# Optimization experiments

Measured on AMD Instinct MI355X. Metric: run time of the kernel, lower is better.

The kernel has to match this reference:

```python
import jax, jax.numpy as jnp
import numpy as np

N_NODES = 100000
N_EDGES = 1200000
D = 64          # hidden_feat_dim == out_feat_dim
D_CELL = 16     # cell_feat_dim
HID = 256       # MLP hidden width (from MLP(..., 256, ...))
N_TGT = 50000


def setup_inputs() -> dict:
    key = jax.random.key(0)
    ks = jax.random.split(key, 13)
    inv = lambda d: 1.0 / np.sqrt(d)
    return {
        "h": jax.random.normal(ks[0], (N_NODES, D), jnp.float32),
        "cell_feat": jax.random.normal(ks[1], (N_NODES, D_CELL), jnp.float32),
        "src": jax.random.randint(ks[2], (N_EDGES,), 0, N_NODES, jnp.int32),
        "dst": jax.random.randint(ks[3], (N_EDGES,), 0, N_NODES, jnp.int32),
        "targets": jax.random.randint(ks[4], (N_TGT,), 0, N_NODES, jnp.int32),
        "Wn1": jax.random.normal(ks[5], (D, HID), jnp.float32) * inv(D),
        "bn1": jnp.zeros((HID,), jnp.float32),
        "Wn2": jax.random.normal(ks[6], (HID, D), jnp.float32) * inv(HID),
        "bn2": jnp.zeros((D,), jnp.float32),
        "Ws1": jax.random.normal(ks[7], (D_CELL, HID), jnp.float32) * inv(D_CELL),
        "bs1": jnp.zeros((HID,), jnp.float32),
        "Ws2": jax.random.normal(ks[8], (HID, D), jnp.float32) * inv(HID),
        "bs2": jnp.zeros((D,), jnp.float32),
    }


def _mlp2(x, W1, b1, W2, b2):
    # MLP(d_in, 256, d_out) with LeakyReLU(negative_slope=0) == ReLU
    return jax.nn.relu(x @ W1 + b1) @ W2 + b2


def reference(h, cell_feat, src, dst, targets,
              Wn1, bn1, Wn2, bn2, Ws1, bs1, Ws2, bs2):
    # PathConv forward, even level_id > 0, flag_attn=False:
    #   pull(copy_src('h','m'), cell_msg_reduce, apply_cell_func) on 'cell' edges
    N = h.shape[0]
    m = h[src]  # gather edge messages [E, D]
    # cell_msg_reduce: per-dst, per-channel softmax over incoming messages
    mmax = jax.ops.segment_max(m, dst, num_segments=N)          # [N, D]
    mmax = jnp.where(jnp.isfinite(mmax), mmax, 0.0)             # isolated nodes
    e = jnp.exp(m - mmax[dst])                                  # [E, D]
    den = jax.ops.segment_sum(e, dst, num_segments=N)           # [N, D]
    num = jax.ops.segment_sum(e * m, dst, num_segments=N)       # sum(msg*softmax)
    h_neigh1 = num / jnp.where(den == 0.0, 1.0, den)            # [N, D]
    # apply_cell_func: fc_cell_self(cell_feat) + fc_cell_neigh(h_neigh1)
    h_new = _mlp2(cell_feat, Ws1, bs1, Ws2, bs2) + _mlp2(h_neigh1, Wn1, bn1, Wn2, bn2)
    h_new = jax.nn.relu(h_new)  # self.activation
    return h_new[targets]
```

## Files before the change

kernel.cpp:

```cpp
#include <hip/hip_runtime.h>

#define NN 100000
#define NE 1200000
#define DD 64
#define DC 16
#define DH 256
#define NT 50000
#define MAXDEG 64

typedef __attribute__((ext_vector_type(8))) short bf16x8;
typedef __attribute__((ext_vector_type(4))) short bf16x4;
typedef __attribute__((ext_vector_type(4))) float f32x4;

__device__ __forceinline__ unsigned short f2bf(float x) {
    unsigned int u = __float_as_uint(x);
    return (unsigned short)((u + 0x7FFFu + ((u >> 16) & 1u)) >> 16);
}
__device__ __forceinline__ float bf2f(unsigned short b) {
    return __uint_as_float(((unsigned int)b) << 16);
}

__device__ __forceinline__ void split8t(const float* p, bf16x8& hi, bf16x8& lo) {
    f32x4 a = *reinterpret_cast<const f32x4*>(p);
    f32x4 b = *reinterpret_cast<const f32x4*>(p + 4);
    #pragma unroll
    for (int j = 0; j < 4; ++j) {
        unsigned short h = (unsigned short)(__float_as_uint(a[j]) >> 16);
        hi[j] = (short)h;
        lo[j] = (short)(__float_as_uint(a[j] - bf2f(h)) >> 16);
    }
    #pragma unroll
    for (int j = 0; j < 4; ++j) {
        unsigned short h = (unsigned short)(__float_as_uint(b[j]) >> 16);
        hi[4 + j] = (short)h;
        lo[4 + j] = (short)(__float_as_uint(b[j] - bf2f(h)) >> 16);
    }
}

__device__ __forceinline__ bf16x8 zero8() {
    return bf16x8{0, 0, 0, 0, 0, 0, 0, 0};
}
__device__ __forceinline__ bf16x8 pad8(bf16x4 v) {
    return bf16x8{v[0], v[1], v[2], v[3], 0, 0, 0, 0};
}

#define N_W1NT 16384
#define N_W1ST 8192
#define N_W2N  16384
#define N_W2S  16384
#define N_PACK (N_W1NT + N_W1ST + N_W2N + N_W2S)
#define N_PREP NN

__global__ __launch_bounds__(256) void prep_k(
    const float* __restrict__ Wn1, const float* __restrict__ Ws1,
    const float* __restrict__ Wn2, const float* __restrict__ Ws2,
    unsigned short* __restrict__ W1nT, unsigned short* __restrict__ W1sT,
    unsigned short* __restrict__ W2n,  unsigned short* __restrict__ W2s,
    int* __restrict__ ifl, int* __restrict__ deg)
{
    int tid = blockIdx.x * 256 + threadIdx.x;
    if (tid < NN) ifl[tid] = -1;
    if (tid < NT + 16) deg[tid] = 0;
    if (tid >= N_PACK) return;
    float v; unsigned short* ph; int idx;
    if (tid < N_W1NT) {
        idx = tid;
        int j = idx & 7, l = (idx >> 3) & 63, rest = idx >> 9;
        int ks = rest & 1, c = rest >> 1;
        int feat = ks * 32 + ((l >> 4) << 3) + j, hid = (c << 4) + (l & 15);
        v = Wn1[(size_t)feat * DH + hid];
        ph = W1nT;
    } else if (tid < N_W1NT + N_W1ST) {
        idx = tid - N_W1NT;
        int j = idx & 7, l = (idx >> 3) & 63, c = idx >> 9;
        int k = ((l >> 4) << 3) + j, hid = (c << 4) + (l & 15);
        v = (k < DC) ? Ws1[(size_t)k * DH + hid] : 0.0f;
        ph = W1sT;
    } else if (tid < N_W1NT + N_W1ST + N_W2N) {
        idx = tid - N_W1NT - N_W1ST;
        int j = idx & 3, l = (idx >> 2) & 63, rest = idx >> 8;
        int u = rest & 3, c = rest >> 2;
        int row = (c << 4) + ((l >> 4) << 2) + j, col = (u << 4) + (l & 15);
        v = Wn2[(size_t)row * DD + col];
        ph = W2n;
    } else {
        idx = tid - N_W1NT - N_W1ST - N_W2N;
        int j = idx & 3, l = (idx >> 2) & 63, rest = idx >> 8;
        int u = rest & 3, c = rest >> 2;
        int row = (c << 4) + ((l >> 4) << 2) + j, col = (u << 4) + (l & 15);
        v = Ws2[(size_t)row * DD + col];
        ph = W2s;
    }
    ph[idx] = f2bf(v);
}

__global__ __launch_bounds__(256) void mark_wl_k(
    const int* __restrict__ tg, int* __restrict__ ifl, int* __restrict__ cnt)
{
    int i = blockIdx.x * 256 + threadIdx.x;
    int lane = threadIdx.x & 63;
    bool claim = false;
    int t = 0;
    if (i < NT) {
        t = tg[i];
        claim = (atomicCAS(&ifl[t], -1, -2) == -1);
    }
    unsigned long long mask = __ballot(claim);
    if (mask == 0ull) return;
    int nclaim = __popcll(mask);
    int leader = __ffsll((unsigned long long)mask) - 1;
    int base = 0;
    if (lane == leader) base = atomicAdd(cnt, nclaim);
    base = __shfl(base, leader);
    if (claim) {
        int rank = __popcll(mask & ((1ull << lane) - 1ull));
        ifl[t] = base + rank;
    }
}

#define NE4 (NE / 4)
#define N_SCAT (NE4 > NT ? NE4 : NT)

__global__ __launch_bounds__(256) void scatter_tgw_k(
    const int4* __restrict__ src4, const int4* __restrict__ dst4,
    const int* __restrict__ ifl, const int* __restrict__ tg,
    int* __restrict__ tgw, int* __restrict__ deg, int* __restrict__ csr)
{
    int tid = blockIdx.x * 256 + threadIdx.x;
    if (tid < NE4) {
        int4 d = dst4[tid];
        int4 s = src4[tid];
        int w;
        w = ifl[d.x]; if (w >= 0) { int sl = atomicAdd(&deg[w], 1); if (sl < MAXDEG) csr[w * MAXDEG + sl] = s.x; }
        w = ifl[d.y]; if (w >= 0) { int sl = atomicAdd(&deg[w], 1); if (sl < MAXDEG) csr[w * MAXDEG + sl] = s.y; }
        w = ifl[d.z]; if (w >= 0) { int sl = atomicAdd(&deg[w], 1); if (sl < MAXDEG) csr[w * MAXDEG + sl] = s.z; }
        w = ifl[d.w]; if (w >= 0) { int sl = atomicAdd(&deg[w], 1); if (sl < MAXDEG) csr[w * MAXDEG + sl] = s.w; }
    }
    if (tid < NT) tgw[tid] = ifl[tg[tid]];
}

__global__ __launch_bounds__(256) void reduce_k(
    const float* __restrict__ h, const int* __restrict__ csr,
    const int* __restrict__ deg, const int* __restrict__ cnt,
    float* __restrict__ hn_c)
{
    int gw = (blockIdx.x * 256 + threadIdx.x) >> 6;
    int lane = threadIdx.x & 63;
    if (gw >= cnt[0]) return;
    int g = min(deg[gw], MAXDEG);
    int sid = csr[gw * MAXDEG + lane];
    if (lane >= g) sid = 0;
    const int e4 = lane >> 4, c4 = lane & 15;

    f32x4 accd = {0.f, 0.f, 0.f, 0.f}, accn = {0.f, 0.f, 0.f, 0.f};
    for (int base = 0; base < g; base += 16) {
        f32x4 m[4];
        bool  val[4];
        #pragma unroll
        for (int bb = 0; bb < 4; ++bb) {
            int idx = base + bb * 4 + e4;
            val[bb] = (idx < g);
            if (base + bb * 4 < g) {
                int s = __shfl(sid, idx);
                m[bb] = *reinterpret_cast<const f32x4*>(
                            h + (size_t)s * DD + c4 * 4);
            } else {
                m[bb] = f32x4{0.f, 0.f, 0.f, 0.f};
                val[bb] = false;
            }
        }
        #pragma unroll
        for (int bb = 0; bb < 4; ++bb) {
            #pragma unroll
            for (int r = 0; r < 4; ++r) {
                float ex = __expf(m[bb][r]);
                ex = val[bb] ? ex : 0.f;
                accd[r] += ex;
                accn[r] = fmaf(ex, m[bb][r], accn[r]);
            }
        }
    }
    #pragma unroll
    for (int r = 0; r < 4; ++r) {
        accd[r] += __shfl_xor(accd[r], 16);
        accn[r] += __shfl_xor(accn[r], 16);
        accd[r] += __shfl_xor(accd[r], 32);
        accn[r] += __shfl_xor(accn[r], 32);
    }
    if (lane < 16) {
        f32x4 o;
        #pragma unroll
        for (int r = 0; r < 4; ++r)
            o[r] = (accd[r] == 0.f) ? 0.f : accn[r] / accd[r];
        *reinterpret_cast<f32x4*>(hn_c + (size_t)gw * DD + c4 * 4) = o;
    }
}

__global__ __launch_bounds__(256, 4) void mfma_mlp_k(
    const float* __restrict__ hn_c, const int* __restrict__ tgw,
    const float* __restrict__ cellf, const int* __restrict__ tg,
    const unsigned short* __restrict__ W1nT, const unsigned short* __restrict__ W1sT,
    const unsigned short* __restrict__ W2n,  const unsigned short* __restrict__ W2s,
    const float* __restrict__ bn1, const float* __restrict__ bs1,
    const float* __restrict__ bn2, const float* __restrict__ bs2,
    float* __restrict__ out)
{
    __shared__ float shbuf[4 * 16 * 68];
    float (*X)[84]      = reinterpret_cast<float(*)[84]>(shbuf);
    float (*Ys)[16][68] = reinterpret_cast<float(*)[16][68]>(shbuf);

    const int tid = threadIdx.x;
    const int wv = tid >> 6, ln = tid & 63;
    const int l16 = ln & 15, kb = (ln >> 4) << 3;
    const int rbase = blockIdx.x * 32;

    {
        int r = tid >> 3, seg = tid & 7;
        int row = rbase + r; if (row >= NT) row = NT - 1;
        int w = tgw[row];
        const float* hp = hn_c + (size_t)w * DD + seg * 8;
        *reinterpret_cast<f32x4*>(&X[r][seg * 8])     = *reinterpret_cast<const f32x4*>(hp);
        *reinterpret_cast<f32x4*>(&X[r][seg * 8 + 4]) = *reinterpret_cast<const f32x4*>(hp + 4);
        if (tid < 128) {
            int r2 = tid >> 2, q = tid & 3;
            int row2 = rbase + r2; if (row2 >= NT) row2 = NT - 1;
            int t2 = tg[row2];
            *reinterpret_cast<f32x4*>(&X[r2][64 + q * 4]) =
                *reinterpret_cast<const f32x4*>(cellf + (size_t)t2 * DC + q * 4);
        }
    }
    __syncthreads();

    bf16x8 xh[2][2], xl[2][2], sxh[2], sxl[2];
    #pragma unroll
    for (int g = 0; g < 2; ++g) {
        #pragma unroll
        for (int ks = 0; ks < 2; ++ks)
            split8t(&X[g * 16 + l16][ks * 32 + kb], xh[g][ks], xl[g][ks]);
        sxh[g] = zero8(); sxl[g] = zero8();
        if (ln < 32)
            split8t(&X[g * 16 + l16][64 + kb], sxh[g], sxl[g]);
    }
    __syncthreads();

    f32x4 accY[2][4];
    #pragma unroll
    for (int g = 0; g < 2; ++g)
        #pragma unroll
        for (int u = 0; u < 4; ++u) accY[g][u] = f32x4{0.f, 0.f, 0.f, 0.f};

    #pragma unroll
    for (int cc = 0; cc < 4; ++cc) {
        int cg = (wv << 2) + cc;
        f32x4 b1 = *reinterpret_cast<const f32x4*>(bn1 + cg * 16 + ((ln >> 4) << 2));
        f32x4 a1[2] = {b1, b1};
        #pragma unroll
        for (int ks = 0; ks < 2; ++ks) {
            bf16x8 wh = *reinterpret_cast<const bf16x8*>(W1nT + (((cg * 2 + ks) * 64 + ln) << 3));
            #pragma unroll
            for (int g = 0; g < 2; ++g) {
                a1[g] = __builtin_amdgcn_mfma_f32_16x16x32_bf16(wh, xh[g][ks], a1[g], 0, 0, 0);
                a1[g] = __builtin_amdgcn_mfma_f32_16x16x32_bf16(wh, xl[g][ks], a1[g], 0, 0, 0);
            }
        }
        bf16x8 pah[2], pal[2];
        #pragma unroll
        for (int g = 0; g < 2; ++g) {
            pah[g] = zero8(); pal[g] = zero8();
            #pragma unroll
            for (int r = 0; r < 4; ++r) {
                float d = fmaxf(a1[g][r], 0.f);
                unsigned short hh = (unsigned short)(__float_as_uint(d) >> 16);
                pah[g][r] = (short)hh;
                pal[g][r] = (short)(__float_as_uint(d - bf2f(hh)) >> 16);
            }
        }
        #pragma unroll
        for (int u = 0; u < 4; ++u) {
            bf16x8 wp = pad8(*reinterpret_cast<const bf16x4*>(W2n + (((cg * 4 + u) * 64 + ln) << 2)));
            #pragma unroll
            for (int g = 0; g < 2; ++g) {
                accY[g][u] = __builtin_amdgcn_mfma_f32_16x16x32_bf16(pah[g], wp, accY[g][u], 0, 0, 0);
                accY[g][u] = __builtin_amdgcn_mfma_f32_16x16x32_bf16(pal[g], wp, accY[g][u], 0, 0, 0);
            }
        }
    }

    #pragma unroll
    for (int cc = 0; cc < 4; ++cc) {
        int cg = (wv << 2) + cc;
        f32x4 b1 = *reinterpret_cast<const f32x4*>(bs1 + cg * 16 + ((ln >> 4) << 2));
        f32x4 a1[2] = {b1, b1};
        {
            bf16x8 wh = *reinterpret_cast<const bf16x8*>(W1sT + ((cg * 64 + ln) << 3));
            #pragma unroll
            for (int g = 0; g < 2; ++g) {
                a1[g] = __builtin_amdgcn_mfma_f32_16x16x32_bf16(wh, sxh[g], a1[g], 0, 0, 0);
                a1[g] = __builtin_amdgcn_mfma_f32_16x16x32_bf16(wh, sxl[g], a1[g], 0, 0, 0);
            }
        }
        bf16x8 pah[2], pal[2];
        #pragma unroll
        for (int g = 0; g < 2; ++g) {
            pah[g] = zero8(); pal[g] = zero8();
            #pragma unroll
            for (int r = 0; r < 4; ++r) {
                float d = fmaxf(a1[g][r], 0.f);
                unsigned short hh = (unsigned short)(__float_as_uint(d) >> 16);
                pah[g][r] = (short)hh;
                pal[g][r] = (short)(__float_as_uint(d - bf2f(hh)) >> 16);
            }
        }
        #pragma unroll
        for (int u = 0; u < 4; ++u) {
            bf16x8 wp = pad8(*reinterpret_cast<const bf16x4*>(W2s + (((cg * 4 + u) * 64 + ln) << 2)));
            #pragma unroll
            for (int g = 0; g < 2; ++g) {
                accY[g][u] = __builtin_amdgcn_mfma_f32_16x16x32_bf16(pah[g], wp, accY[g][u], 0, 0, 0);
                accY[g][u] = __builtin_amdgcn_mfma_f32_16x16x32_bf16(pal[g], wp, accY[g][u], 0, 0, 0);
            }
        }
    }

    #pragma unroll
    for (int g = 0; g < 2; ++g) {
        #pragma unroll
        for (int u = 0; u < 4; ++u)
            #pragma unroll
            for (int r = 0; r < 4; ++r)
                Ys[wv][(ln >> 4) * 4 + r][u * 16 + l16] = accY[g][u][r];
        __syncthreads();
        {
            int row = tid >> 4, cs = tid & 15;
            f32x4 s = {0.f, 0.f, 0.f, 0.f};
            #pragma unroll
            for (int wq = 0; wq < 4; ++wq)
                s += *reinterpret_cast<const f32x4*>(&Ys[wq][row][cs * 4]);
            f32x4 c0 = *reinterpret_cast<const f32x4*>(bn2 + cs * 4);
            f32x4 c1 = *reinterpret_cast<const f32x4*>(bs2 + cs * 4);
            #pragma unroll
            for (int j = 0; j < 4; ++j) s[j] = fmaxf(s[j] + c0[j] + c1[j], 0.f);
            int rowg = rbase + g * 16 + row;
            if (rowg < NT)
                *reinterpret_cast<f32x4*>(out + (size_t)rowg * DD + cs * 4) = s;
        }
        __syncthreads();
    }
}

extern "C" void kernel_launch(void* const* d_in, const int* in_sizes, int n_in,
                              void* d_out, int out_size, void* d_ws, size_t ws_size,
                              hipStream_t stream)
{
    const float* h     = (const float*)d_in[0];
    const float* cellf = (const float*)d_in[1];
    const int*   src   = (const int*)d_in[2];
    const int*   dst   = (const int*)d_in[3];
    const int*   tg    = (const int*)d_in[4];
    const float* Wn1   = (const float*)d_in[5];
    const float* bn1   = (const float*)d_in[6];
    const float* Wn2   = (const float*)d_in[7];
    const float* bn2   = (const float*)d_in[8];
    const float* Ws1   = (const float*)d_in[9];
    const float* bs1   = (const float*)d_in[10];
    const float* Ws2   = (const float*)d_in[11];
    const float* bs2   = (const float*)d_in[12];
    float* out = (float*)d_out;

    int*   ifl  = (int*)d_ws;
    int*   deg  = ifl + NN;
    int*   cnt  = deg + NT;
    int*   tgw  = cnt + 16;
    int*   csr  = tgw + NT;
    float* hn_c = (float*)(csr + (size_t)NT * MAXDEG);
    size_t woff = ((size_t)((char*)(hn_c + (size_t)NT * DD) - (char*)d_ws) + 63)
                  & ~(size_t)63;
    unsigned short* W1nT = (unsigned short*)((char*)d_ws + woff);
    unsigned short* W1sT = W1nT + N_W1NT;
    unsigned short* W2n  = W1sT + N_W1ST;
    unsigned short* W2s  = W2n + N_W2N;

    prep_k<<<(N_PREP + 255) / 256, 256, 0, stream>>>(
        Wn1, Ws1, Wn2, Ws2, W1nT, W1sT, W2n, W2s, ifl, deg);

    mark_wl_k<<<(NT + 255) / 256, 256, 0, stream>>>(tg, ifl, cnt);

    scatter_tgw_k<<<(N_SCAT + 255) / 256, 256, 0, stream>>>(
        (const int4*)src, (const int4*)dst, ifl, tg, tgw, deg, csr);

    reduce_k<<<NT / 4, 256, 0, stream>>>(h, csr, deg, cnt, hn_c);

    mfma_mlp_k<<<(NT + 31) / 32, 256, 0, stream>>>(hn_c, tgw, cellf, tg,
        W1nT, W1sT, W2n, W2s, bn1, bs1, bn2, bs2, out);
}
```

Baseline: 97.22 us.

## Give each wave its own 16 rows across full hidden width in MLP kernel

The MLP kernel used to split the 256-wide hidden dimension across four waves, with each wave covering all 32 rows of the block, and then reduce the partial outputs through shared memory with extra barriers. Now each wave owns 16 rows and loops over all 16 hidden chunks for both MLPs, so it writes its output directly with no cross-wave reduction and no Ys buffer. Blocks cover 64 rows instead of 32, which halves the grid. The trade-off is that each wave now loads all of W1/W2 itself, which raises weight-load traffic per row, and output stores become scalar strided writes instead of vectorized ones.

```diff
diff --git a/kernel.cpp b/kernel.cpp
--- a/kernel.cpp
+++ b/kernel.cpp
@@ -196,6 +196,8 @@
     }
 }
 
+#define NT64 ((NT + 63) / 64)
+
 __global__ __launch_bounds__(256, 4) void mfma_mlp_k(
     const float* __restrict__ hn_c, const int* __restrict__ tgw,
     const float* __restrict__ cellf, const int* __restrict__ tg,
@@ -205,146 +207,93 @@
     const float* __restrict__ bn2, const float* __restrict__ bs2,
     float* __restrict__ out)
 {
-    __shared__ float shbuf[4 * 16 * 68];
-    float (*X)[84]      = reinterpret_cast<float(*)[84]>(shbuf);
-    float (*Ys)[16][68] = reinterpret_cast<float(*)[16][68]>(shbuf);
+    __shared__ float X[64][84];
 
     const int tid = threadIdx.x;
     const int wv = tid >> 6, ln = tid & 63;
     const int l16 = ln & 15, kb = (ln >> 4) << 3;
-    const int rbase = blockIdx.x * 32;
+    const int rbase = blockIdx.x * 64;
 
     {
-        int r = tid >> 3, seg = tid & 7;
+        int r = tid >> 2, seg = tid & 3;
         int row = rbase + r; if (row >= NT) row = NT - 1;
         int w = tgw[row];
-        const float* hp = hn_c + (size_t)w * DD + seg * 8;
-        *reinterpret_cast<f32x4*>(&X[r][seg * 8])     = *reinterpret_cast<const f32x4*>(hp);
-        *reinterpret_cast<f32x4*>(&X[r][seg * 8 + 4]) = *reinterpret_cast<const f32x4*>(hp + 4);
-        if (tid < 128) {
-            int r2 = tid >> 2, q = tid & 3;
-            int row2 = rbase + r2; if (row2 >= NT) row2 = NT - 1;
-            int t2 = tg[row2];
-            *reinterpret_cast<f32x4*>(&X[r2][64 + q * 4]) =
-                *reinterpret_cast<const f32x4*>(cellf + (size_t)t2 * DC + q * 4);
-        }
+        const float* hp = hn_c + (size_t)w * DD + seg * 16;
+        *reinterpret_cast<f32x4*>(&X[r][seg * 16])      = *reinterpret_cast<const f32x4*>(hp);
+        *reinterpret_cast<f32x4*>(&X[r][seg * 16 + 4])  = *reinterpret_cast<const f32x4*>(hp + 4);
+        *reinterpret_cast<f32x4*>(&X[r][seg * 16 + 8])  = *reinterpret_cast<const f32x4*>(hp + 8);
+        *reinterpret_cast<f32x4*>(&X[r][seg * 16 + 12]) = *reinterpret_cast<const f32x4*>(hp + 12);
+        int t2 = tg[row];
+        *reinterpret_cast<f32x4*>(&X[r][64 + seg * 4]) =
+            *reinterpret_cast<const f32x4*>(cellf + (size_t)t2 * DC + seg * 4);
     }
     __syncthreads();
 
-    bf16x8 xh[2][2], xl[2][2], sxh[2], sxl[2];
-    #pragma unroll
-    for (int g = 0; g < 2; ++g) {
-        #pragma unroll
-        for (int ks = 0; ks < 2; ++ks)
-            split8t(&X[g * 16 + l16][ks * 32 + kb], xh[g][ks], xl[g][ks]);
-        sxh[g] = zero8(); sxl[g] = zero8();
-        if (ln < 32)
-            split8t(&X[g * 16 + l16][64 + kb], sxh[g], sxl[g]);
-    }
-    __syncthreads();
-
-    f32x4 accY[2][4];
-    #pragma unroll
-    for (int g = 0; g < 2; ++g)
-        #pragma unroll
-        for (int u = 0; u < 4; ++u) accY[g][u] = f32x4{0.f, 0.f, 0.f, 0.f};
-
-    #pragma unroll
-    for (int cc = 0; cc < 4; ++cc) {
-        int cg = (wv << 2) + cc;
-        f32x4 b1 = *reinterpret_cast<const f32x4*>(bn1 + cg * 16 + ((ln >> 4) << 2));
-        f32x4 a1[2] = {b1, b1};
+    bf16x8 xh[2], xl[2], sxh, sxl;
+    #pragma unroll
+    for (int ks = 0; ks < 2; ++ks)
+        split8t(&X[wv * 16 + l16][ks * 32 + kb], xh[ks], xl[ks]);
+    sxh = zero8(); sxl = zero8();
+    if (ln < 32)
+        split8t(&X[wv * 16 + l16][64 + kb], sxh, sxl);
+
+    f32x4 accY[4];
+    #pragma unroll
+    for (int u = 0; u < 4; ++u) accY[u] = f32x4{0.f, 0.f, 0.f, 0.f};
+
+    #pragma unroll
+    for (int cg = 0; cg < 16; ++cg) {
+        f32x4 a1 = *reinterpret_cast<const f32x4*>(bn1 + cg * 16 + ((ln >> 4) << 2));
         #pragma unroll
         for (int ks = 0; ks < 2; ++ks) {
             bf16x8 wh = *reinterpret_cast<const bf16x8*>(W1nT + (((cg * 2 + ks) * 64 + ln) << 3));
-            #pragma unroll
-            for (int g = 0; g < 2; ++g) {
-                a1[g] = __builtin_amdgcn_mfma_f32_16x16x32_bf16(wh, xh[g][ks], a1[g], 0, 0, 0);
-                a1[g] = __builtin_amdgcn_mfma_f32_16x16x32_bf16(wh, xl[g][ks], a1[g], 0, 0, 0);
-            }
-        }
-        bf16x8 pah[2], pal[2];
-        #pragma unroll
-        for (int g = 0; g < 2; ++g) {
-            pah[g] = zero8(); pal[g] = zero8();
+            a1 = __builtin_amdgcn_mfma_f32_16x16x32_bf16(wh, xh[ks], a1, 0, 0, 0);
+            a1 = __builtin_amdgcn_mfma_f32_16x16x32_bf16(wh, xl[ks], a1, 0, 0, 0);
+        }
+        f32x4 a1s = *reinterpret_cast<const f32x4*>(bs1 + cg * 16 + ((ln >> 4) << 2));
+        {
+            bf16x8 whs = *reinterpret_cast<const bf16x8*>(W1sT + ((cg * 64 + ln) << 3));
+            a1s = __builtin_amdgcn_mfma_f32_16x16x32_bf16(whs, sxh, a1s, 0, 0, 0);
+            a1s = __builtin_amdgcn_mfma_f32_16x16x32_bf16(whs, sxl, a1s, 0, 0, 0);
+        }
+        bf16x8 pah = zero8(), pal = zero8(), psh = zero8(), psl = zero8();
+        #pragma unroll
+        for (int r = 0; r < 4; ++r) {
+            float d = fmaxf(a1[r], 0.f);
+            unsigned short hh = (unsigned short)(__float_as_uint(d) >> 16);
+            pah[r] = (short)hh;
+            pal[r] = (short)(__float_as_uint(d - bf2f(hh)) >> 16);
+            float ds = fmaxf(a1s[r], 0.f);
+            unsigned short hs = (unsigned short)(__float_as_uint(ds) >> 16);
+            psh[r] = (short)hs;
+            psl[r] = (short)(__float_as_uint(ds - bf2f(hs)) >> 16);
+        }
+        #pragma unroll
+        for (int u = 0; u < 4; ++u) {
+            bf16x8 wpn = pad8(*reinterpret_cast<const bf16x4*>(W2n + (((cg * 4 + u) * 64 + ln) << 2)));
+            accY[u] = __builtin_amdgcn_mfma_f32_16x16x32_bf16(pah, wpn, accY[u], 0, 0, 0);
+            accY[u] = __builtin_amdgcn_mfma_f32_16x16x32_bf16(pal, wpn, accY[u], 0, 0, 0);
+            bf16x8 wps = pad8(*reinterpret_cast<const bf16x4*>(W2s + (((cg * 4 + u) * 64 + ln) << 2)));
+            accY[u] = __builtin_amdgcn_mfma_f32_16x16x32_bf16(psh, wps, accY[u], 0, 0, 0);
+            accY[u] = __builtin_amdgcn_mfma_f32_16x16x32_bf16(psl, wps, accY[u], 0, 0, 0);
+        }
+    }
+
+    {
+        const int s4 = (ln >> 4) << 2;
+        float b2[4];
+        #pragma unroll
+        for (int u = 0; u < 4; ++u)
+            b2[u] = bn2[u * 16 + l16] + bs2[u * 16 + l16];
+        #pragma unroll
+        for (int u = 0; u < 4; ++u)
             #pragma unroll
             for (int r = 0; r < 4; ++r) {
-                float d = fmaxf(a1[g][r], 0.f);
-                unsigned short hh = (unsigned short)(__float_as_uint(d) >> 16);
-                pah[g][r] = (short)hh;
-                pal[g][r] = (short)(__float_as_uint(d - bf2f(hh)) >> 16);
+                int rowg = rbase + wv * 16 + s4 + r;
+                if (rowg < NT)
+                    out[(size_t)rowg * DD + u * 16 + l16] =
+                        fmaxf(accY[u][r] + b2[u], 0.f);
             }
-        }
-        #pragma unroll
-        for (int u = 0; u < 4; ++u) {
-            bf16x8 wp = pad8(*reinterpret_cast<const bf16x4*>(W2n + (((cg * 4 + u) * 64 + ln) << 2)));
-            #pragma unroll
-            for (int g = 0; g < 2; ++g) {
-                accY[g][u] = __builtin_amdgcn_mfma_f32_16x16x32_bf16(pah[g], wp, accY[g][u], 0, 0, 0);
-                accY[g][u] = __builtin_amdgcn_mfma_f32_16x16x32_bf16(pal[g], wp, accY[g][u], 0, 0, 0);
-            }
-        }
-    }
-
-    #pragma unroll
-    for (int cc = 0; cc < 4; ++cc) {
-        int cg = (wv << 2) + cc;
-        f32x4 b1 = *reinterpret_cast<const f32x4*>(bs1 + cg * 16 + ((ln >> 4) << 2));
-        f32x4 a1[2] = {b1, b1};
-        {
-            bf16x8 wh = *reinterpret_cast<const bf16x8*>(W1sT + ((cg * 64 + ln) << 3));
-            #pragma unroll
-            for (int g = 0; g < 2; ++g) {
-                a1[g] = __builtin_amdgcn_mfma_f32_16x16x32_bf16(wh, sxh[g], a1[g], 0, 0, 0);
-                a1[g] = __builtin_amdgcn_mfma_f32_16x16x32_bf16(wh, sxl[g], a1[g], 0, 0, 0);
-            }
-        }
-        bf16x8 pah[2], pal[2];
-        #pragma unroll
-        for (int g = 0; g < 2; ++g) {
-            pah[g] = zero8(); pal[g] = zero8();
-            #pragma unroll
-            for (int r = 0; r < 4; ++r) {
-                float d = fmaxf(a1[g][r], 0.f);
-                unsigned short hh = (unsigned short)(__float_as_uint(d) >> 16);
-                pah[g][r] = (short)hh;
-                pal[g][r] = (short)(__float_as_uint(d - bf2f(hh)) >> 16);
-            }
-        }
-        #pragma unroll
-        for (int u = 0; u < 4; ++u) {
-            bf16x8 wp = pad8(*reinterpret_cast<const bf16x4*>(W2s + (((cg * 4 + u) * 64 + ln) << 2)));
-            #pragma unroll
-            for (int g = 0; g < 2; ++g) {
-                accY[g][u] = __builtin_amdgcn_mfma_f32_16x16x32_bf16(pah[g], wp, accY[g][u], 0, 0, 0);
-                accY[g][u] = __builtin_amdgcn_mfma_f32_16x16x32_bf16(pal[g], wp, accY[g][u], 0, 0, 0);
-            }
-        }
-    }
-
-    #pragma unroll
-    for (int g = 0; g < 2; ++g) {
-        #pragma unroll
-        for (int u = 0; u < 4; ++u)
-            #pragma unroll
-            for (int r = 0; r < 4; ++r)
-                Ys[wv][(ln >> 4) * 4 + r][u * 16 + l16] = accY[g][u][r];
-        __syncthreads();
-        {
-            int row = tid >> 4, cs = tid & 15;
-            f32x4 s = {0.f, 0.f, 0.f, 0.f};
-            #pragma unroll
-            for (int wq = 0; wq < 4; ++wq)
-                s += *reinterpret_cast<const f32x4*>(&Ys[wq][row][cs * 4]);
-            f32x4 c0 = *reinterpret_cast<const f32x4*>(bn2 + cs * 4);
-            f32x4 c1 = *reinterpret_cast<const f32x4*>(bs2 + cs * 4);
-            #pragma unroll
-            for (int j = 0; j < 4; ++j) s[j] = fmaxf(s[j] + c0[j] + c1[j], 0.f);
-            int rowg = rbase + g * 16 + row;
-            if (rowg < NT)
-                *reinterpret_cast<f32x4*>(out + (size_t)rowg * DD + cs * 4) = s;
-        }
-        __syncthreads();
     }
 }
 
@@ -390,6 +339,6 @@
 
     reduce_k<<<NT / 4, 256, 0, stream>>>(h, csr, deg, cnt, hn_c);
 
-    mfma_mlp_k<<<(NT + 31) / 32, 256, 0, stream>>>(hn_c, tgw, cellf, tg,
+    mfma_mlp_k<<<NT64, 256, 0, stream>>>(hn_c, tgw, cellf, tg,
         W1nT, W1sT, W2n, W2s, bn1, bs1, bn2, bs2, out);
 }
```

Result: slower. 99.78 us (+2.6%).
